# Kernel tuning notes

Measured on AMD Instinct MI355X. Metric: run time of the kernel, lower is better.

The kernel has to match this reference:

```python
import jax, jax.numpy as jnp
import numpy as np


def setup_inputs() -> dict:
    key = jax.random.key(0)
    k1, k2 = jax.random.split(key)
    outputs = jax.random.normal(k1, (8192, 64), dtype=jnp.float32)
    labels = jax.random.randint(k2, (8192,), 0, 10)
    return {"outputs": outputs, "labels": labels}


def reference(outputs, labels):
    # outputs: [b, d], labels: [b]
    # Original: distances[i, j] = sqrt(||o_i - o_j||_2) * (-1 if labels differ else 5)
    # for j > i, then summed. sqrt(norm) == (sum of squared diffs) ** 0.25.
    b = outputs.shape[0]
    sq = jnp.sum(outputs * outputs, axis=1)                      # [b]
    gram = outputs @ outputs.T                                   # [b, b]
    d2 = jnp.maximum(sq[:, None] + sq[None, :] - 2.0 * gram, 0.0)  # squared L2 dists
    upper = jnp.triu(jnp.ones((b, b), dtype=bool), k=1)          # j > i mask
    factor = jnp.where(labels[:, None] != labels[None, :], -1.0, 5.0)
    d2_safe = jnp.where(upper, d2, 1.0)                          # avoid 0**0.25 grad issues
    dist = d2_safe ** 0.25                                       # sqrt(L2 norm)
    return jnp.sum(jnp.where(upper, dist * factor, 0.0))
```

## Files before the change

### kernel.cpp

```cpp
#include <hip/hip_runtime.h>


typedef __bf16 bf16x8 __attribute__((ext_vector_type(8)));
typedef float  f32x4  __attribute__((ext_vector_type(4)));
typedef int    i32x4  __attribute__((ext_vector_type(4)));

#define BT    128
#define DK    64
#define LSTR  72
#define PANEL (128 * LSTR)

__device__ __forceinline__ float qroot(float x) {
    return __builtin_amdgcn_sqrtf(__builtin_amdgcn_sqrtf(x));
}
__device__ __forceinline__ unsigned short rne_bf16(float v) {
    const unsigned u = __builtin_bit_cast(unsigned, v);
    return (unsigned short)((u + 0x7fffu + ((u >> 16) & 1u)) >> 16);
}

__global__ __launch_bounds__(256)
void ss_prep(const float* __restrict__ O, unsigned short* __restrict__ Obf,
             float* __restrict__ sqb) {
    const int row  = blockIdx.x * 4 + (threadIdx.x >> 6);
    const int lane = threadIdx.x & 63;
    const float v = O[(size_t)row * 64 + lane];
    const unsigned short w = rne_bf16(v);
    Obf[(size_t)row * 64 + lane] = w;
    const float wf = __builtin_bit_cast(float, (unsigned)w << 16);
    float s = wf * wf;
    #pragma unroll
    for (int off = 32; off; off >>= 1) s += __shfl_xor(s, off);
    if (lane == 0) sqb[row] = s;
}

__global__ __launch_bounds__(256, 4)
void ss_mfma(const unsigned short* __restrict__ Obf, const float* __restrict__ sqb,
             const int* __restrict__ L, float* __restrict__ partials, int nt) {
    const int t = blockIdx.x;
    const float fnt = (float)nt + 0.5f;
    int ti = (int)floorf(fnt - sqrtf(fnt * fnt - 2.0f * (float)t));
    if (ti < 0) ti = 0;
    if (ti > nt - 1) ti = nt - 1;
    while (ti > 0 && ti * nt - (ti * (ti - 1)) / 2 > t) --ti;
    while ((ti + 1) * nt - ((ti + 1) * ti) / 2 <= t) ++ti;
    const int tj = ti + (t - (ti * nt - (ti * (ti - 1)) / 2));

    const int tid  = threadIdx.x;
    const int wave = tid >> 6, lane = tid & 63;
    const int wr = wave >> 1, wc = wave & 1;
    const bool diag = (ti == tj);

    __shared__ unsigned short lds[2 * PANEL];
    __shared__ float wsum[4];

    {
        const unsigned short* srcA = Obf + (size_t)(ti * BT) * DK;
        const unsigned short* srcB = Obf + (size_t)(tj * BT) * DK;
        bf16x8 ra[4], rb[4];
        #pragma unroll
        for (int k = 0; k < 4; ++k) {
            const int id = k * 256 + tid;
            ra[k] = *(const bf16x8*)(srcA + id * 8);
            rb[k] = *(const bf16x8*)(srcB + id * 8);
        }
        #pragma unroll
        for (int k = 0; k < 4; ++k) {
            const int id  = k * 256 + tid;
            const int row = id >> 3, col = id & 7;
            *(bf16x8*)(&lds[row * LSTR + col * 8])         = ra[k];
            *(bf16x8*)(&lds[PANEL + row * LSTR + col * 8]) = rb[k];
        }
    }
    __syncthreads();

    const int lrow = lane & 15;
    const int kq   = lane >> 4;
    const int r0   = ti * BT + wr * 64;

    float accs = 0.0f;

    if (!(diag && (wc < wr))) {
        f32x4 sqi[4]; i32x4 li[4];
        #pragma unroll
        for (int f = 0; f < 4; ++f) {
            const int ib = r0 + f * 16 + (kq << 2);
            sqi[f] = *(const f32x4*)(sqb + ib);
            li[f]  = *(const i32x4*)(L + ib);
        }
        const bool masked = diag && (wr == wc);

        bf16x8 afr[4][2];
        #pragma unroll
        for (int i = 0; i < 4; ++i) {
            const unsigned short* pa = &lds[(wr * 64 + i * 16 + lrow) * LSTR + kq * 8];
            afr[i][0] = *(const bf16x8*)pa;
            afr[i][1] = *(const bf16x8*)(pa + 32);
        }

        #pragma unroll
        for (int jh = 0; jh < 2; ++jh) {
            bf16x8 bfr[2][2];
            #pragma unroll
            for (int g = 0; g < 2; ++g) {
                const unsigned short* pb =
                    &lds[PANEL + (wc * 64 + jh * 32 + g * 16 + lrow) * LSTR + kq * 8];
                bfr[g][0] = *(const bf16x8*)pb;
                bfr[g][1] = *(const bf16x8*)(pb + 32);
            }

            f32x4 acc[4][2];
            #pragma unroll
            for (int i = 0; i < 4; ++i)
                #pragma unroll
                for (int g = 0; g < 2; ++g)
                    acc[i][g] = (f32x4){0.f, 0.f, 0.f, 0.f};

            #pragma unroll
            for (int i = 0; i < 4; ++i)
                #pragma unroll
                for (int g = 0; g < 2; ++g) {
                    acc[i][g] = __builtin_amdgcn_mfma_f32_16x16x32_bf16(afr[i][0], bfr[g][0], acc[i][g], 0, 0, 0);
                    acc[i][g] = __builtin_amdgcn_mfma_f32_16x16x32_bf16(afr[i][1], bfr[g][1], acc[i][g], 0, 0, 0);
                }

            const int c0 = tj * BT + wc * 64 + jh * 32;
            #pragma unroll
            for (int g = 0; g < 2; ++g) {
                const int j    = c0 + g * 16 + lrow;
                const float sj = sqb[j];
                const int  ljv = L[j];
                if (masked) {
                    #pragma unroll
                    for (int fi = 0; fi < 4; ++fi) {
                        const int ib = r0 + fi * 16 + (kq << 2);
                        #pragma unroll
                        for (int r = 0; r < 4; ++r) {
                            float d2 = fmaf(-2.0f, acc[fi][g][r], sqi[fi][r] + sj);
                            d2 = fmaxf(d2, 0.0f);
                            const float dist = qroot(d2);
                            const float fac  = (li[fi][r] != ljv) ? -1.0f : 5.0f;
                            accs += (j > ib + r) ? dist * fac : 0.0f;
                        }
                    }
                } else {
                    #pragma unroll
                    for (int fi = 0; fi < 4; ++fi) {
                        #pragma unroll
                        for (int r = 0; r < 4; ++r) {
                            float d2 = fmaf(-2.0f, acc[fi][g][r], sqi[fi][r] + sj);
                            d2 = fmaxf(d2, 0.0f);
                            const float dist = qroot(d2);
                            const float fac  = (li[fi][r] != ljv) ? -1.0f : 5.0f;
                            accs = fmaf(dist, fac, accs);
                        }
                    }
                }
            }
        }
    }

    #pragma unroll
    for (int off = 32; off > 0; off >>= 1) accs += __shfl_down(accs, off);
    if (lane == 0) wsum[wave] = accs;
    __syncthreads();
    if (tid == 0) partials[t] = (wsum[0] + wsum[1]) + (wsum[2] + wsum[3]);
}

__global__ void ss_reduce_kernel(const float* __restrict__ partials, int n,
                                 float* __restrict__ out) {
    __shared__ float s[4];
    const int tid = threadIdx.x;
    float acc = 0.0f;
    for (int idx = tid; idx < n; idx += 256) acc += partials[idx];
    #pragma unroll
    for (int off = 32; off > 0; off >>= 1) acc += __shfl_down(acc, off);
    if ((tid & 63) == 0) s[tid >> 6] = acc;
    __syncthreads();
    if (tid == 0) out[0] = (s[0] + s[1]) + (s[2] + s[3]);
}

extern "C" void kernel_launch(void* const* d_in, const int* in_sizes, int n_in,
                              void* d_out, int out_size, void* d_ws, size_t ws_size,
                              hipStream_t stream) {
    const float* O = (const float*)d_in[0];
    const int*   L = (const int*)d_in[1];
    float* out = (float*)d_out;

    const int b    = in_sizes[1];
    const int nt   = b / BT;
    const int ntri = nt * (nt + 1) / 2;

    char* ws = (char*)d_ws;
    float*          partials = (float*)ws;
    float*          sqb      = (float*)(ws + (64 << 10));
    unsigned short* Obf      = (unsigned short*)(ws + (128 << 10));

    ss_prep<<<b / 4, 256, 0, stream>>>(O, Obf, sqb);
    ss_mfma<<<ntri, 256, 0, stream>>>(Obf, sqb, L, partials, nt);
    ss_reduce_kernel<<<1, 256, 0, stream>>>(partials, ntri, out);
}
```

Measured before the change: 28.79 us.

## Process two triangular tiles per block with prefetch of next tile panels

Each block now handles two consecutive upper-triangular tiles, prefetching the next tile's B panel (and A panel only if the row changes) into registers while computing the current one. This halves the block count, amortises launch and index math, and overlaps global loads with MFMA and epilogue work. Launch bounds drop from 4 to 3 waves-per-EU hint to allow more registers for the prefetch buffers. It assumes ntri is even (nt=64 gives 2080), otherwise the last tile would be dropped.

New measurement: 32.35 us. 12.4% more time.

```diff
diff --git a/kernel.cpp b/kernel.cpp
--- a/kernel.cpp
+++ b/kernel.cpp
@@ -33,125 +33,149 @@
     if (lane == 0) sqb[row] = s;
 }
 
-__global__ __launch_bounds__(256, 4)
+__global__ __launch_bounds__(256, 3)
 void ss_mfma(const unsigned short* __restrict__ Obf, const float* __restrict__ sqb,
              const int* __restrict__ L, float* __restrict__ partials, int nt) {
-    const int t = blockIdx.x;
-    const float fnt = (float)nt + 0.5f;
-    int ti = (int)floorf(fnt - sqrtf(fnt * fnt - 2.0f * (float)t));
-    if (ti < 0) ti = 0;
-    if (ti > nt - 1) ti = nt - 1;
-    while (ti > 0 && ti * nt - (ti * (ti - 1)) / 2 > t) --ti;
-    while ((ti + 1) * nt - ((ti + 1) * ti) / 2 <= t) ++ti;
-    const int tj = ti + (t - (ti * nt - (ti * (ti - 1)) / 2));
-
     const int tid  = threadIdx.x;
     const int wave = tid >> 6, lane = tid & 63;
     const int wr = wave >> 1, wc = wave & 1;
-    const bool diag = (ti == tj);
+    const int lrow = lane & 15;
+    const int kq   = lane >> 4;
+
+    const int t0 = blockIdx.x * 2;
+    const float fnt = (float)nt + 0.5f;
+    int ti = (int)floorf(fnt - sqrtf(fnt * fnt - 2.0f * (float)t0));
+    if (ti < 0) ti = 0;
+    if (ti > nt - 1) ti = nt - 1;
+    while (ti > 0 && ti * nt - (ti * (ti - 1)) / 2 > t0) --ti;
+    while ((ti + 1) * nt - ((ti + 1) * ti) / 2 <= t0) ++ti;
+    int tj = ti + (t0 - (ti * nt - (ti * (ti - 1)) / 2));
 
     __shared__ unsigned short lds[2 * PANEL];
     __shared__ float wsum[4];
 
+    bf16x8 ra[4], rb[4];
     {
         const unsigned short* srcA = Obf + (size_t)(ti * BT) * DK;
         const unsigned short* srcB = Obf + (size_t)(tj * BT) * DK;
-        bf16x8 ra[4], rb[4];
         #pragma unroll
         for (int k = 0; k < 4; ++k) {
             const int id = k * 256 + tid;
             ra[k] = *(const bf16x8*)(srcA + id * 8);
             rb[k] = *(const bf16x8*)(srcB + id * 8);
         }
+    }
+    bool wrA = true;
+
+    float accs = 0.0f;
+
+    #pragma unroll
+    for (int q = 0; q < 2; ++q) {
+        __syncthreads();
         #pragma unroll
         for (int k = 0; k < 4; ++k) {
             const int id  = k * 256 + tid;
             const int row = id >> 3, col = id & 7;
-            *(bf16x8*)(&lds[row * LSTR + col * 8])         = ra[k];
+            if (wrA) *(bf16x8*)(&lds[row * LSTR + col * 8]) = ra[k];
             *(bf16x8*)(&lds[PANEL + row * LSTR + col * 8]) = rb[k];
         }
-    }
-    __syncthreads();
-
-    const int lrow = lane & 15;
-    const int kq   = lane >> 4;
-    const int r0   = ti * BT + wr * 64;
-
-    float accs = 0.0f;
-
-    if (!(diag && (wc < wr))) {
-        f32x4 sqi[4]; i32x4 li[4];
-        #pragma unroll
-        for (int f = 0; f < 4; ++f) {
-            const int ib = r0 + f * 16 + (kq << 2);
-            sqi[f] = *(const f32x4*)(sqb + ib);
-            li[f]  = *(const i32x4*)(L + ib);
-        }
-        const bool masked = diag && (wr == wc);
-
-        bf16x8 afr[4][2];
-        #pragma unroll
-        for (int i = 0; i < 4; ++i) {
-            const unsigned short* pa = &lds[(wr * 64 + i * 16 + lrow) * LSTR + kq * 8];
-            afr[i][0] = *(const bf16x8*)pa;
-            afr[i][1] = *(const bf16x8*)(pa + 32);
-        }
-
-        #pragma unroll
-        for (int jh = 0; jh < 2; ++jh) {
-            bf16x8 bfr[2][2];
-            #pragma unroll
-            for (int g = 0; g < 2; ++g) {
-                const unsigned short* pb =
-                    &lds[PANEL + (wc * 64 + jh * 32 + g * 16 + lrow) * LSTR + kq * 8];
-                bfr[g][0] = *(const bf16x8*)pb;
-                bfr[g][1] = *(const bf16x8*)(pb + 32);
-            }
-
-            f32x4 acc[4][2];
-            #pragma unroll
-            for (int i = 0; i < 4; ++i)
-                #pragma unroll
-                for (int g = 0; g < 2; ++g)
-                    acc[i][g] = (f32x4){0.f, 0.f, 0.f, 0.f};
-
-            #pragma unroll
-            for (int i = 0; i < 4; ++i)
+        __syncthreads();
+
+        const int Cti = ti, Ctj = tj;
+
+        if (q == 0) {
+            int nti = ti, ntj = tj + 1;
+            if (ntj == nt) { nti = ti + 1; ntj = nti; }
+            wrA = (nti != ti);
+            const unsigned short* srcB = Obf + (size_t)(ntj * BT) * DK;
+            #pragma unroll
+            for (int k = 0; k < 4; ++k)
+                rb[k] = *(const bf16x8*)(srcB + (k * 256 + tid) * 8);
+            if (wrA) {
+                const unsigned short* srcA = Obf + (size_t)(nti * BT) * DK;
+                #pragma unroll
+                for (int k = 0; k < 4; ++k)
+                    ra[k] = *(const bf16x8*)(srcA + (k * 256 + tid) * 8);
+            }
+            ti = nti; tj = ntj;
+        }
+
+        const bool diag = (Cti == Ctj);
+        const int r0 = Cti * BT + wr * 64;
+        if (!(diag && (wc < wr))) {
+            f32x4 sqi[4]; i32x4 li[4];
+            #pragma unroll
+            for (int f = 0; f < 4; ++f) {
+                const int ib = r0 + f * 16 + (kq << 2);
+                sqi[f] = *(const f32x4*)(sqb + ib);
+                li[f]  = *(const i32x4*)(L + ib);
+            }
+            const bool masked = diag && (wr == wc);
+
+            bf16x8 afr[4][2];
+            #pragma unroll
+            for (int i = 0; i < 4; ++i) {
+                const unsigned short* pa = &lds[(wr * 64 + i * 16 + lrow) * LSTR + kq * 8];
+                afr[i][0] = *(const bf16x8*)pa;
+                afr[i][1] = *(const bf16x8*)(pa + 32);
+            }
+
+            #pragma unroll
+            for (int jh = 0; jh < 2; ++jh) {
+                bf16x8 bfr[2][2];
                 #pragma unroll
                 for (int g = 0; g < 2; ++g) {
-                    acc[i][g] = __builtin_amdgcn_mfma_f32_16x16x32_bf16(afr[i][0], bfr[g][0], acc[i][g], 0, 0, 0);
-                    acc[i][g] = __builtin_amdgcn_mfma_f32_16x16x32_bf16(afr[i][1], bfr[g][1], acc[i][g], 0, 0, 0);
+                    const unsigned short* pb =
+                        &lds[PANEL + (wc * 64 + jh * 32 + g * 16 + lrow) * LSTR + kq * 8];
+                    bfr[g][0] = *(const bf16x8*)pb;
+                    bfr[g][1] = *(const bf16x8*)(pb + 32);
                 }
 
-            const int c0 = tj * BT + wc * 64 + jh * 32;
-            #pragma unroll
-            for (int g = 0; g < 2; ++g) {
-                const int j    = c0 + g * 16 + lrow;
-                const float sj = sqb[j];
-                const int  ljv = L[j];
-                if (masked) {
+                f32x4 acc[4][2];
+                #pragma unroll
+                for (int i = 0; i < 4; ++i)
                     #pragma unroll
-                    for (int fi = 0; fi < 4; ++fi) {
-                        const int ib = r0 + fi * 16 + (kq << 2);
+                    for (int g = 0; g < 2; ++g)
+                        acc[i][g] = (f32x4){0.f, 0.f, 0.f, 0.f};
+
+                #pragma unroll
+                for (int i = 0; i < 4; ++i)
+                    #pragma unroll
+                    for (int g = 0; g < 2; ++g) {
+                        acc[i][g] = __builtin_amdgcn_mfma_f32_16x16x32_bf16(afr[i][0], bfr[g][0], acc[i][g], 0, 0, 0);
+                        acc[i][g] = __builtin_amdgcn_mfma_f32_16x16x32_bf16(afr[i][1], bfr[g][1], acc[i][g], 0, 0, 0);
+                    }
+
+                const int c0 = Ctj * BT + wc * 64 + jh * 32;
+                #pragma unroll
+                for (int g = 0; g < 2; ++g) {
+                    const int j    = c0 + g * 16 + lrow;
+                    const float sj = sqb[j];
+                    const int  ljv = L[j];
+                    if (masked) {
                         #pragma unroll
-                        for (int r = 0; r < 4; ++r) {
-                            float d2 = fmaf(-2.0f, acc[fi][g][r], sqi[fi][r] + sj);
-                            d2 = fmaxf(d2, 0.0f);
-                            const float dist = qroot(d2);
-                            const float fac  = (li[fi][r] != ljv) ? -1.0f : 5.0f;
-                            accs += (j > ib + r) ? dist * fac : 0.0f;
+                        for (int fi = 0; fi < 4; ++fi) {
+                            const int ib = r0 + fi * 16 + (kq << 2);
+                            #pragma unroll
+                            for (int r = 0; r < 4; ++r) {
+                                float d2 = fmaf(-2.0f, acc[fi][g][r], sqi[fi][r] + sj);
+                                d2 = fmaxf(d2, 0.0f);
+                                const float dist = qroot(d2);
+                                const float fac  = (li[fi][r] != ljv) ? -1.0f : 5.0f;
+                                accs += (j > ib + r) ? dist * fac : 0.0f;
+                            }
                         }
-                    }
-                } else {
-                    #pragma unroll
-                    for (int fi = 0; fi < 4; ++fi) {
+                    } else {
                         #pragma unroll
-                        for (int r = 0; r < 4; ++r) {
-                            float d2 = fmaf(-2.0f, acc[fi][g][r], sqi[fi][r] + sj);
-                            d2 = fmaxf(d2, 0.0f);
-                            const float dist = qroot(d2);
-                            const float fac  = (li[fi][r] != ljv) ? -1.0f : 5.0f;
-                            accs = fmaf(dist, fac, accs);
+                        for (int fi = 0; fi < 4; ++fi) {
+                            #pragma unroll
+                            for (int r = 0; r < 4; ++r) {
+                                float d2 = fmaf(-2.0f, acc[fi][g][r], sqi[fi][r] + sj);
+                                d2 = fmaxf(d2, 0.0f);
+                                const float dist = qroot(d2);
+                                const float fac  = (li[fi][r] != ljv) ? -1.0f : 5.0f;
+                                accs = fmaf(dist, fac, accs);
+                            }
                         }
                     }
                 }
@@ -163,7 +187,7 @@
     for (int off = 32; off > 0; off >>= 1) accs += __shfl_down(accs, off);
     if (lane == 0) wsum[wave] = accs;
     __syncthreads();
-    if (tid == 0) partials[t] = (wsum[0] + wsum[1]) + (wsum[2] + wsum[3]);
+    if (tid == 0) partials[blockIdx.x] = (wsum[0] + wsum[1]) + (wsum[2] + wsum[3]);
 }
 
 __global__ void ss_reduce_kernel(const float* __restrict__ partials, int n,
@@ -189,6 +213,7 @@
     const int b    = in_sizes[1];
     const int nt   = b / BT;
     const int ntri = nt * (nt + 1) / 2;
+    const int nblk = ntri / 2;
 
     char* ws = (char*)d_ws;
     float*          partials = (float*)ws;
@@ -196,6 +221,6 @@
     unsigned short* Obf      = (unsigned short*)(ws + (128 << 10));
 
     ss_prep<<<b / 4, 256, 0, stream>>>(O, Obf, sqb);
-    ss_mfma<<<ntri, 256, 0, stream>>>(Obf, sqb, L, partials, nt);
-    ss_reduce_kernel<<<1, 256, 0, stream>>>(partials, ntri, out);
-}
+    ss_mfma<<<nblk, 256, 0, stream>>>(Obf, sqb, L, partials, nt);
+    ss_reduce_kernel<<<1, 256, 0, stream>>>(partials, nblk, out);
+}
```
